# Optimization experiments

Measured on AMD Instinct MI355X. Metric: run time of the kernel, lower is better.

The kernel has to match this reference:

```python
import jax, jax.numpy as jnp
import numpy as np

N = 50000; E = 1600000; F_IN = 32; HEADS = 8; D = 16; HID = HEADS * D
ED = 16; G = 512; MH = 512; MO = 512; SLOPE = 0.2


def setup_inputs() -> dict:
    key = jax.random.key(0)
    ks = jax.random.split(key, 40)
    inp = {}
    inp["x"] = jax.random.normal(ks[0], (N, F_IN), jnp.float32)
    inp["edge_index"] = jax.random.randint(ks[1], (2, E), 0, N)
    inp["edge_attr"] = jax.random.normal(ks[2], (E, ED), jnp.float32)
    inp["batch"] = jnp.sort(jax.random.randint(ks[3], (N,), 0, G))

    def lin(k, fi, fo):
        return jax.random.normal(k, (fi, fo), jnp.float32) / np.sqrt(fi).astype(np.float32)

    i = 4
    dims = [(F_IN, HID), (HID, HID), (HID, HID)]  # GATv2 layers 0..2
    for l, (fi, fo) in enumerate(dims):
        inp[f"Wl{l}"] = lin(ks[i], fi, fo); i += 1
        inp[f"bl{l}"] = jnp.zeros((fo,), jnp.float32)
        inp[f"Wr{l}"] = lin(ks[i], fi, fo); i += 1
        inp[f"br{l}"] = jnp.zeros((fo,), jnp.float32)
        inp[f"We{l}"] = lin(ks[i], ED, fo); i += 1
        inp[f"att{l}"] = jax.random.normal(ks[i], (HEADS, D), jnp.float32) / np.sqrt(D).astype(np.float32); i += 1
        inp[f"b{l}"] = jnp.zeros((fo,), jnp.float32)
    inp["mW1"] = lin(ks[i], HID, MH); i += 1
    inp["mb1"] = jnp.zeros((MH,), jnp.float32)
    inp["ln_g"] = jnp.ones((MH,), jnp.float32)
    inp["ln_b"] = jnp.zeros((MH,), jnp.float32)
    inp["mW2"] = lin(ks[i], MH, MO); i += 1
    inp["mb2"] = jnp.zeros((MO,), jnp.float32)
    return inp


def _gatv2(h, src, dst, ea, Wl, bl, Wr, br, We, att, b):
    # One GATv2Conv layer (eval mode, add_self_loops already applied).
    n = h.shape[0]
    xl = (h @ Wl + bl).reshape(n, HEADS, D)   # source transform
    xr = (h @ Wr + br).reshape(n, HEADS, D)   # target transform
    ee = (ea @ We).reshape(-1, HEADS, D)      # edge transform (no bias in PyG)
    m = xl[src] + xr[dst] + ee                # [E', H, D]
    m = jnp.where(m > 0, m, SLOPE * m)        # LeakyReLU(0.2)
    s = jnp.einsum('ehd,hd->eh', m, att)      # attention logits
    mx = jax.ops.segment_max(s, dst, num_segments=n)
    ex = jnp.exp(s - mx[dst])
    den = jax.ops.segment_sum(ex, dst, num_segments=n)
    alpha = ex / den[dst]                     # softmax over incoming edges
    out = jax.ops.segment_sum(alpha[:, :, None] * xl[src], dst, num_segments=n)
    return out.reshape(n, HEADS * D) + b


def _forward(x, edge_index, edge_attr, batch,
             Wl0, bl0, Wr0, br0, We0, att0, b0,
             Wl1, bl1, Wr1, br1, We1, att1, b1,
             Wl2, bl2, Wr2, br2, We2, att2, b2,
             mW1, mb1, ln_g, ln_b, mW2, mb2):
    src, dst = edge_index[0], edge_index[1]
    # add_self_loops with fill_value='mean': self-loop edge_attr = mean of incoming edge_attr
    cnt = jax.ops.segment_sum(jnp.ones((E,), jnp.float32), dst, num_segments=N)
    loop_attr = jax.ops.segment_sum(edge_attr, dst, num_segments=N) / jnp.clip(cnt, 1.0)[:, None]
    nodes = jnp.arange(N)
    src_f = jnp.concatenate([src, nodes])
    dst_f = jnp.concatenate([dst, nodes])
    ea = jnp.concatenate([edge_attr, loop_attr], axis=0)

    h = jax.nn.relu(_gatv2(x, src_f, dst_f, ea, Wl0, bl0, Wr0, br0, We0, att0, b0))
    h = jax.nn.relu(_gatv2(h, src_f, dst_f, ea, Wl1, bl1, Wr1, br1, We1, att1, b1))
    h = _gatv2(h, src_f, dst_f, ea, Wl2, bl2, Wr2, br2, We2, att2, b2)

    g = jax.ops.segment_sum(h, batch, num_segments=G)  # sum pooling per graph
    z = jax.nn.relu(g @ mW1 + mb1)
    mu = jnp.mean(z, axis=-1, keepdims=True)
    var = jnp.var(z, axis=-1, keepdims=True)
    z = (z - mu) / jnp.sqrt(var + 1e-5) * ln_g + ln_b
    return z @ mW2 + mb2


def reference(x, edge_index, edge_attr, batch,
              Wl0, bl0, Wr0, br0, We0, att0, b0,
              Wl1, bl1, Wr1, br1, We1, att1, b1,
              Wl2, bl2, Wr2, br2, We2, att2, b2,
              mW1, mb1, ln_g, ln_b, mW2, mb2):
    return _forward(x, edge_index, edge_attr, batch,
                    Wl0, bl0, Wr0, br0, We0, att0, b0,
                    Wl1, bl1, Wr1, br1, We1, att1, b1,
                    Wl2, bl2, Wr2, br2, We2, att2, b2,
                    mW1, mb1, ln_g, ln_b, mW2, mb2)
```

## Files before the change

kernel.cpp:

```cpp
#include <hip/hip_runtime.h>
#include <math.h>

#define NN 50000
#define EE 1600000
#define FIN 32
#define HID_ 128
#define ED_ 16
#define GG 512
#define MH_ 512
#define MO_ 512

typedef float v2f __attribute__((ext_vector_type(2)));

#if __has_builtin(__builtin_amdgcn_exp2f)
#define EXP2(x) __builtin_amdgcn_exp2f(x)
#else
#define EXP2(x) exp2f(x)
#endif

template <int CTRL>
__device__ __forceinline__ float dpp_add(float x) {
  int m = __builtin_amdgcn_update_dpp(0, __float_as_int(x), CTRL, 0xF, 0xF, true);
  return x + __int_as_float(m);
}

__device__ __forceinline__ float bfly8(float p) {
  p = dpp_add<0xB1>(p);
  p = dpp_add<0x4E>(p);
  p = dpp_add<0x141>(p);
  return p;
}


__global__ void hist_kernel(const int4* __restrict__ dst4, int* __restrict__ cnt) {
  int e = blockIdx.x * 256 + threadIdx.x;
  if (e >= EE / 4) return;
  int4 d = dst4[e];
  atomicAdd(&cnt[d.x], 1);
  atomicAdd(&cnt[d.y], 1);
  atomicAdd(&cnt[d.z], 1);
  atomicAdd(&cnt[d.w], 1);
}

__global__ __launch_bounds__(256) void scan1_kernel(const int* __restrict__ in, int n,
                                                    int* __restrict__ out,
                                                    int* __restrict__ bsums) {
  int chunk = blockIdx.x;
  int base = chunk * 1024;
  int t = threadIdx.x;
  int idx = base + t * 4;
  int v0 = (idx + 0 < n) ? in[idx + 0] : 0;
  int v1 = (idx + 1 < n) ? in[idx + 1] : 0;
  int v2 = (idx + 2 < n) ? in[idx + 2] : 0;
  int v3 = (idx + 3 < n) ? in[idx + 3] : 0;
  int ts = v0 + v1 + v2 + v3;
  int lane = t & 63, w = t >> 6;
  int s = ts;
#pragma unroll
  for (int off = 1; off < 64; off <<= 1) {
    int o = __shfl_up(s, off);
    if (lane >= off) s += o;
  }
  __shared__ int wsum[4];
  if (lane == 63) wsum[w] = s;
  __syncthreads();
  int woff = 0;
  for (int i = 0; i < w; i++) woff += wsum[i];
  int excl = woff + s - ts;
  int run = excl;
  run += v0; if (idx + 0 < n) out[idx + 0] = run;
  run += v1; if (idx + 1 < n) out[idx + 1] = run;
  run += v2; if (idx + 2 < n) out[idx + 2] = run;
  run += v3; if (idx + 3 < n) out[idx + 3] = run;
  if (t == 255) bsums[chunk] = woff + s;
}

__global__ void scan_add_kernel(int* __restrict__ rowptr, const int* __restrict__ bscan, int n) {
  int i = blockIdx.x * 256 + threadIdx.x;
  if (i == 0) rowptr[0] = 0;
  if (i < n) {
    int chunk = i >> 10;
    if (chunk > 0) rowptr[1 + i] += bscan[chunk - 1];
  }
}

__global__ void scatter_kernel(const int4* __restrict__ src4, const int4* __restrict__ dst4,
                               const int* __restrict__ rowptr, int* __restrict__ fill,
                               int2* __restrict__ csr) {
  int e = blockIdx.x * 256 + threadIdx.x;
  if (e >= EE / 4) return;
  int4 s = src4[e];
  int4 d = dst4[e];
  int eb = e * 4;
  int p0 = rowptr[d.x] + atomicAdd(&fill[d.x], 1);
  csr[p0] = make_int2(s.x, eb + 0);
  int p1 = rowptr[d.y] + atomicAdd(&fill[d.y], 1);
  csr[p1] = make_int2(s.y, eb + 1);
  int p2 = rowptr[d.z] + atomicAdd(&fill[d.z], 1);
  csr[p2] = make_int2(s.z, eb + 2);
  int p3 = rowptr[d.w] + atomicAdd(&fill[d.w], 1);
  csr[p3] = make_int2(s.w, eb + 3);
}

__global__ __launch_bounds__(256) void loopattr_kernel(const int* __restrict__ rowptr,
                                                       const int2* __restrict__ csr,
                                                       const float* __restrict__ ea,
                                                       float* __restrict__ la) {
  int wid = threadIdx.x >> 6, lane = threadIdx.x & 63;
  int v = __builtin_amdgcn_readfirstlane(blockIdx.x * 4 + wid);
  if (v >= NN) return;
  int s = __builtin_amdgcn_readfirstlane(rowptr[v]);
  int e = __builtin_amdgcn_readfirstlane(rowptr[v + 1]);
  int k = lane >> 4;
  int d = lane & 15;
  float acc = 0.f;
  for (int j = s + k; j < e; j += 4) acc += ea[(size_t)csr[j].y * 16 + d];
  acc += __shfl_xor(acc, 16);
  acc += __shfl_xor(acc, 32);
  if (lane < 16) la[(size_t)v * 16 + d] = (e > s) ? acc / (float)(e - s) : 0.f;
}


template <int F>
__global__ __launch_bounds__(256) void node_transform(const float* __restrict__ h,
                                                      const float* __restrict__ Wlm,
                                                      const float* __restrict__ blm,
                                                      const float* __restrict__ Wrm,
                                                      const float* __restrict__ brm,
                                                      float* __restrict__ xl,
                                                      float* __restrict__ xr, int nnodes) {
  __shared__ float hs[F * 32];
  int v0 = blockIdx.x * 32;
  int t = threadIdx.x;
  for (int idx = t; idx < 32 * F; idx += 256) {
    int i = idx / F, k = idx - i * F;
    hs[k * 32 + i] = (v0 + i < nnodes) ? h[(size_t)(v0 + i) * F + k] : 0.f;
  }
  __syncthreads();
  bool isL = t < 128;
  int q = t & 63;
  int nh = (t >> 6) & 1;
  const float* Wm = isL ? Wlm : Wrm;
  v2f acc[16];
#pragma unroll
  for (int i = 0; i < 16; i++) acc[i] = (v2f){0.f, 0.f};
  for (int k = 0; k < F; k++) {
    v2f w = *(const v2f*)(Wm + k * 128 + 2 * q);
    const float4* hk4 = (const float4*)(hs + k * 32 + nh * 16);
#pragma unroll
    for (int r = 0; r < 4; r++) {
      float4 hv = hk4[r];
      acc[4 * r + 0] = __builtin_elementwise_fma((v2f){hv.x, hv.x}, w, acc[4 * r + 0]);
      acc[4 * r + 1] = __builtin_elementwise_fma((v2f){hv.y, hv.y}, w, acc[4 * r + 1]);
      acc[4 * r + 2] = __builtin_elementwise_fma((v2f){hv.z, hv.z}, w, acc[4 * r + 2]);
      acc[4 * r + 3] = __builtin_elementwise_fma((v2f){hv.w, hv.w}, w, acc[4 * r + 3]);
    }
  }
  const float* bm = isL ? blm : brm;
  v2f b = *(const v2f*)(bm + 2 * q);
  float* dstp = isL ? xl : xr;
  int base = v0 + nh * 16;
#pragma unroll
  for (int i = 0; i < 16; i++) {
    if (base + i < nnodes)
      *(v2f*)(dstp + (size_t)(base + i) * 128 + 2 * q) = acc[i] + b;
  }
}


__global__ __launch_bounds__(256) void gat_aggregate(
    const float* __restrict__ xl, const float* __restrict__ xr,
    const int* __restrict__ rowptr, const int2* __restrict__ csr,
    const float* __restrict__ ea, const float* __restrict__ la,
    const float* __restrict__ We, const float* __restrict__ att,
    const float* __restrict__ bias, float* __restrict__ hout, int relu) {
  int wid = threadIdx.x >> 6, lane = threadIdx.x & 63;
  int v = __builtin_amdgcn_readfirstlane(blockIdx.x * 4 + wid);
  if (v >= NN) return;
  int c = 2 * lane;
  v2f wec[16];
#pragma unroll
  for (int k = 0; k < 16; k++) wec[k] = *(const v2f*)(We + k * 128 + c);
  const float L2E = 1.44269504088896340736f;
  v2f av = *(const v2f*)(att + c) * L2E;
  v2f xrv = *(const v2f*)(xr + (size_t)v * 128 + c);

  auto score = [&](int u, const float* eaP, v2f& xu) -> float {
    xu = *(const v2f*)(xl + (size_t)u * 128 + c);
    v2f m = xrv + xu;
#pragma unroll
    for (int k = 0; k < 16; k++) {
      float e = eaP[k];
      m = __builtin_elementwise_fma((v2f){e, e}, wec[k], m);
    }
    m = __builtin_elementwise_max(m, 0.2f * m);
    v2f qq = av * m;
    return bfly8(qq.x + qq.y);
  };

  v2f acc;
  float den;
  {
    v2f xu;
    float p = score(v, la + (size_t)v * 16, xu);
    float w = EXP2(p);
    den = w;
    acc = (v2f){w, w} * xu;
  }
  int start = __builtin_amdgcn_readfirstlane(rowptr[v]);
  int end = __builtin_amdgcn_readfirstlane(rowptr[v + 1]);
  int j = start;
  for (; j + 4 <= end; j += 4) {
    int2 e0 = csr[j], e1 = csr[j + 1], e2 = csr[j + 2], e3 = csr[j + 3];
    int u0 = __builtin_amdgcn_readfirstlane(e0.x);
    int u1 = __builtin_amdgcn_readfirstlane(e1.x);
    int u2 = __builtin_amdgcn_readfirstlane(e2.x);
    int u3 = __builtin_amdgcn_readfirstlane(e3.x);
    const float* p0 = ea + (size_t)__builtin_amdgcn_readfirstlane(e0.y) * 16;
    const float* p1 = ea + (size_t)__builtin_amdgcn_readfirstlane(e1.y) * 16;
    const float* p2 = ea + (size_t)__builtin_amdgcn_readfirstlane(e2.y) * 16;
    const float* p3 = ea + (size_t)__builtin_amdgcn_readfirstlane(e3.y) * 16;
    v2f x0, x1, x2, x3;
    float s0 = score(u0, p0, x0);
    float s1 = score(u1, p1, x1);
    float s2 = score(u2, p2, x2);
    float s3 = score(u3, p3, x3);
    float w0 = EXP2(s0), w1 = EXP2(s1), w2 = EXP2(s2), w3 = EXP2(s3);
    den += (w0 + w1) + (w2 + w3);
    acc = __builtin_elementwise_fma((v2f){w0, w0}, x0,
          __builtin_elementwise_fma((v2f){w1, w1}, x1,
          __builtin_elementwise_fma((v2f){w2, w2}, x2,
          __builtin_elementwise_fma((v2f){w3, w3}, x3, acc))));
  }
  for (; j < end; ++j) {
    int2 e0 = csr[j];
    int u = __builtin_amdgcn_readfirstlane(e0.x);
    const float* p0 = ea + (size_t)__builtin_amdgcn_readfirstlane(e0.y) * 16;
    v2f xu;
    float p = score(u, p0, xu);
    float w = EXP2(p);
    den += w;
    acc = __builtin_elementwise_fma((v2f){w, w}, xu, acc);
  }
  float invd = 1.f / den;
  v2f bv = *(const v2f*)(bias + c);
  v2f o = __builtin_elementwise_fma(acc, (v2f){invd, invd}, bv);
  if (relu) o = __builtin_elementwise_max(o, (v2f){0.f, 0.f});
  *(v2f*)(hout + (size_t)v * 128 + c) = o;
}


__global__ void gptr_kernel(const int* __restrict__ batch, int* __restrict__ gptr) {
  int g = blockIdx.x * 256 + threadIdx.x;
  if (g > GG) return;
  int lo = 0, hi = NN;
  while (lo < hi) {
    int mid = (lo + hi) >> 1;
    if (batch[mid] < g) lo = mid + 1; else hi = mid;
  }
  gptr[g] = lo;
}

__global__ void pool_kernel(const float* __restrict__ h, const int* __restrict__ gptr,
                            float* __restrict__ gp) {
  int gi = blockIdx.x;
  int c = threadIdx.x;
  int s = gptr[gi], e = gptr[gi + 1];
  float acc = 0.f;
  for (int v = s; v < e; v++) acc += h[(size_t)v * 128 + c];
  gp[gi * 128 + c] = acc;
}

__global__ __launch_bounds__(256) void mlp1_kernel(const float* __restrict__ gp,
                                                   const float* __restrict__ mW1,
                                                   const float* __restrict__ mb1,
                                                   const float* __restrict__ lng,
                                                   const float* __restrict__ lnb,
                                                   float* __restrict__ z) {
  int row = blockIdx.x;
  int t = threadIdx.x;
  __shared__ float gs[128];
  if (t < 128) gs[t] = gp[row * 128 + t];
  __syncthreads();
  int c0 = t, c1 = t + 256;
  float z0 = 0.f, z1 = 0.f;
  for (int k = 0; k < 128; k++) {
    float gk = gs[k];
    z0 = fmaf(gk, mW1[k * 512 + c0], z0);
    z1 = fmaf(gk, mW1[k * 512 + c1], z1);
  }
  z0 += mb1[c0]; z1 += mb1[c1];
  z0 = fmaxf(z0, 0.f); z1 = fmaxf(z1, 0.f);
  float s = z0 + z1, q = z0 * z0 + z1 * z1;
#pragma unroll
  for (int off = 32; off > 0; off >>= 1) {
    s += __shfl_xor(s, off);
    q += __shfl_xor(q, off);
  }
  __shared__ float red[8];
  int lane = t & 63, w = t >> 6;
  if (lane == 0) { red[w] = s; red[4 + w] = q; }
  __syncthreads();
  float S = red[0] + red[1] + red[2] + red[3];
  float Q = red[4] + red[5] + red[6] + red[7];
  float mu = S / 512.f;
  float var = Q / 512.f - mu * mu;
  float inv = 1.f / sqrtf(var + 1e-5f);
  z[row * 512 + c0] = (z0 - mu) * inv * lng[c0] + lnb[c0];
  z[row * 512 + c1] = (z1 - mu) * inv * lng[c1] + lnb[c1];
}

__global__ __launch_bounds__(256) void mlp2_kernel(const float* __restrict__ z,
                                                   const float* __restrict__ mW2,
                                                   const float* __restrict__ mb2,
                                                   float* __restrict__ out) {
  int row = blockIdx.x;
  int t = threadIdx.x;
  __shared__ float zs[512];
  for (int i = t; i < 512; i += 256) zs[i] = z[row * 512 + i];
  __syncthreads();
  int c0 = t, c1 = t + 256;
  float o0 = 0.f, o1 = 0.f;
  for (int k = 0; k < 512; k++) {
    float zk = zs[k];
    o0 = fmaf(zk, mW2[k * 512 + c0], o0);
    o1 = fmaf(zk, mW2[k * 512 + c1], o1);
  }
  out[row * 512 + c0] = o0 + mb2[c0];
  out[row * 512 + c1] = o1 + mb2[c1];
}


extern "C" void kernel_launch(void* const* d_in, const int* in_sizes, int n_in,
                              void* d_out, int out_size, void* d_ws, size_t ws_size,
                              hipStream_t stream) {
  const float* x = (const float*)d_in[0];
  const int* ei = (const int*)d_in[1];
  const int* srcE = ei;
  const int* dstE = ei + EE;
  const float* ea = (const float*)d_in[2];
  const int* batch = (const int*)d_in[3];
  const float* Wl[3] = {(const float*)d_in[4], (const float*)d_in[11], (const float*)d_in[18]};
  const float* bl[3] = {(const float*)d_in[5], (const float*)d_in[12], (const float*)d_in[19]};
  const float* Wr[3] = {(const float*)d_in[6], (const float*)d_in[13], (const float*)d_in[20]};
  const float* br[3] = {(const float*)d_in[7], (const float*)d_in[14], (const float*)d_in[21]};
  const float* Wek[3] = {(const float*)d_in[8], (const float*)d_in[15], (const float*)d_in[22]};
  const float* attk[3] = {(const float*)d_in[9], (const float*)d_in[16], (const float*)d_in[23]};
  const float* bk[3] = {(const float*)d_in[10], (const float*)d_in[17], (const float*)d_in[24]};
  const float* mW1 = (const float*)d_in[25];
  const float* mb1 = (const float*)d_in[26];
  const float* lng = (const float*)d_in[27];
  const float* lnb = (const float*)d_in[28];
  const float* mW2 = (const float*)d_in[29];
  const float* mb2 = (const float*)d_in[30];
  float* outp = (float*)d_out;

  char* W = (char*)d_ws;
  size_t off = 0;
  auto take = [&](size_t b) -> void* {
    void* p = W + off;
    off += (b + 255) & ~(size_t)255;
    return p;
  };
  int* cnt = (int*)take(NN * 4);
  int* rowptr = (int*)take((NN + 1) * 4);
  int* bsums = (int*)take(64 * 4);
  int* bscan = (int*)take(64 * 4);
  int* dummy = (int*)take(64 * 4);
  int2* csr = (int2*)take((size_t)EE * 8);
  float* la = (float*)take((size_t)NN * 16 * 4);
  float* xl = (float*)take((size_t)NN * HID_ * 4);
  float* xr = (float*)take((size_t)NN * HID_ * 4);
  float* hbuf = (float*)take((size_t)NN * HID_ * 4);
  int* gptr = (int*)take((GG + 1) * 4);
  float* gpool = (float*)take((size_t)GG * HID_ * 4);
  float* z = (float*)take((size_t)GG * MH_ * 4);
  (void)ws_size; (void)n_in; (void)in_sizes; (void)out_size;

  hipMemsetAsync(cnt, 0, NN * 4, stream);
  hist_kernel<<<(EE / 4 + 255) / 256, 256, 0, stream>>>((const int4*)dstE, cnt);
  scan1_kernel<<<49, 256, 0, stream>>>(cnt, NN, rowptr + 1, bsums);
  scan1_kernel<<<1, 256, 0, stream>>>(bsums, 49, bscan, dummy);
  scan_add_kernel<<<(NN + 255) / 256, 256, 0, stream>>>(rowptr, bscan, NN);
  hipMemsetAsync(cnt, 0, NN * 4, stream);
  scatter_kernel<<<(EE / 4 + 255) / 256, 256, 0, stream>>>((const int4*)srcE, (const int4*)dstE,
                                                           rowptr, cnt, csr);
  loopattr_kernel<<<(NN + 3) / 4, 256, 0, stream>>>(rowptr, csr, ea, la);

  for (int l = 0; l < 3; l++) {
    if (l == 0)
      node_transform<FIN><<<(NN + 31) / 32, 256, 0, stream>>>(x, Wl[0], bl[0], Wr[0], br[0],
                                                              xl, xr, NN);
    else
      node_transform<HID_><<<(NN + 31) / 32, 256, 0, stream>>>(hbuf, Wl[l], bl[l], Wr[l], br[l],
                                                               xl, xr, NN);
    gat_aggregate<<<(NN + 3) / 4, 256, 0, stream>>>(xl, xr, rowptr, csr, ea, la,
                                                    Wek[l], attk[l], bk[l], hbuf,
                                                    (l < 2) ? 1 : 0);
  }

  gptr_kernel<<<3, 256, 0, stream>>>(batch, gptr);
  pool_kernel<<<GG, 128, 0, stream>>>(hbuf, gptr, gpool);
  mlp1_kernel<<<GG, 256, 0, stream>>>(gpool, mW1, mb1, lng, lnb, z);
  mlp2_kernel<<<GG, 256, 0, stream>>>(z, mW2, mb2, outp);
}
```

Baseline: 1.013 ms.

## Fuse self-loop edge-attribute mean into first GAT aggregation layer

Removes the separate loopattr kernel. The first-layer aggregation now accumulates the mean of incoming edge attributes while it walks each node's edges, then scores the self-loop last using that mean, which is broadcast via readlane. Later layers read the stored mean. The change also splits the packed v2f math into scalar float arrays and adds asm register pins. This saves one full pass over the CSR and edge attributes, at the cost of extra loads in layer 0 and a different register and instruction schedule.

```diff
diff --git a/kernel.cpp b/kernel.cpp
--- a/kernel.cpp
+++ b/kernel.cpp
@@ -102,24 +102,6 @@
   csr[p3] = make_int2(s.w, eb + 3);
 }
 
-__global__ __launch_bounds__(256) void loopattr_kernel(const int* __restrict__ rowptr,
-                                                       const int2* __restrict__ csr,
-                                                       const float* __restrict__ ea,
-                                                       float* __restrict__ la) {
-  int wid = threadIdx.x >> 6, lane = threadIdx.x & 63;
-  int v = __builtin_amdgcn_readfirstlane(blockIdx.x * 4 + wid);
-  if (v >= NN) return;
-  int s = __builtin_amdgcn_readfirstlane(rowptr[v]);
-  int e = __builtin_amdgcn_readfirstlane(rowptr[v + 1]);
-  int k = lane >> 4;
-  int d = lane & 15;
-  float acc = 0.f;
-  for (int j = s + k; j < e; j += 4) acc += ea[(size_t)csr[j].y * 16 + d];
-  acc += __shfl_xor(acc, 16);
-  acc += __shfl_xor(acc, 32);
-  if (lane < 16) la[(size_t)v * 16 + d] = (e > s) ? acc / (float)(e - s) : 0.f;
-}
-
 
 template <int F>
 __global__ __launch_bounds__(256) void node_transform(const float* __restrict__ h,
@@ -168,45 +150,55 @@
 }
 
 
+template <int LAYER0>
 __global__ __launch_bounds__(256) void gat_aggregate(
     const float* __restrict__ xl, const float* __restrict__ xr,
     const int* __restrict__ rowptr, const int2* __restrict__ csr,
-    const float* __restrict__ ea, const float* __restrict__ la,
+    const float* __restrict__ ea, float* __restrict__ la,
     const float* __restrict__ We, const float* __restrict__ att,
     const float* __restrict__ bias, float* __restrict__ hout, int relu) {
   int wid = threadIdx.x >> 6, lane = threadIdx.x & 63;
   int v = __builtin_amdgcn_readfirstlane(blockIdx.x * 4 + wid);
   if (v >= NN) return;
   int c = 2 * lane;
-  v2f wec[16];
-#pragma unroll
-  for (int k = 0; k < 16; k++) wec[k] = *(const v2f*)(We + k * 128 + c);
+  float wx[16], wy[16];
+#pragma unroll
+  for (int k = 0; k < 16; k++) {
+    wx[k] = We[k * 128 + c];
+    wy[k] = We[k * 128 + c + 1];
+  }
+#pragma unroll
+  for (int k = 0; k < 16; k++) {
+    asm volatile("" : "+v"(wx[k]));
+    asm volatile("" : "+v"(wy[k]));
+  }
   const float L2E = 1.44269504088896340736f;
-  v2f av = *(const v2f*)(att + c) * L2E;
+  float ax = att[c] * L2E, ay = att[c + 1] * L2E;
   v2f xrv = *(const v2f*)(xr + (size_t)v * 128 + c);
+  float xrx = xrv.x, xry = xrv.y;
+  asm volatile("" : "+v"(ax));
+  asm volatile("" : "+v"(ay));
+  asm volatile("" : "+v"(xrx));
+  asm volatile("" : "+v"(xry));
 
   auto score = [&](int u, const float* eaP, v2f& xu) -> float {
     xu = *(const v2f*)(xl + (size_t)u * 128 + c);
-    v2f m = xrv + xu;
+    float mx = xrx + xu.x, my = xry + xu.y;
 #pragma unroll
     for (int k = 0; k < 16; k++) {
       float e = eaP[k];
-      m = __builtin_elementwise_fma((v2f){e, e}, wec[k], m);
+      mx = fmaf(e, wx[k], mx);
+      my = fmaf(e, wy[k], my);
     }
-    m = __builtin_elementwise_max(m, 0.2f * m);
-    v2f qq = av * m;
-    return bfly8(qq.x + qq.y);
+    mx = fmaxf(mx, 0.2f * mx);
+    my = fmaxf(my, 0.2f * my);
+    return bfly8(fmaf(ax, mx, ay * my));
   };
 
-  v2f acc;
-  float den;
-  {
-    v2f xu;
-    float p = score(v, la + (size_t)v * 16, xu);
-    float w = EXP2(p);
-    den = w;
-    acc = (v2f){w, w} * xu;
-  }
+  int d16 = lane & 15;
+  v2f acc = (v2f){0.f, 0.f};
+  float den = 0.f;
+  float la_f = 0.f;
   int start = __builtin_amdgcn_readfirstlane(rowptr[v]);
   int end = __builtin_amdgcn_readfirstlane(rowptr[v + 1]);
   int j = start;
@@ -220,6 +212,7 @@
     const float* p1 = ea + (size_t)__builtin_amdgcn_readfirstlane(e1.y) * 16;
     const float* p2 = ea + (size_t)__builtin_amdgcn_readfirstlane(e2.y) * 16;
     const float* p3 = ea + (size_t)__builtin_amdgcn_readfirstlane(e3.y) * 16;
+    if (LAYER0) la_f += (p0[d16] + p1[d16]) + (p2[d16] + p3[d16]);
     v2f x0, x1, x2, x3;
     float s0 = score(u0, p0, x0);
     float s1 = score(u1, p1, x1);
@@ -236,12 +229,39 @@
     int2 e0 = csr[j];
     int u = __builtin_amdgcn_readfirstlane(e0.x);
     const float* p0 = ea + (size_t)__builtin_amdgcn_readfirstlane(e0.y) * 16;
+    if (LAYER0) la_f += p0[d16];
     v2f xu;
     float p = score(u, p0, xu);
     float w = EXP2(p);
     den += w;
     acc = __builtin_elementwise_fma((v2f){w, w}, xu, acc);
   }
+
+  int deg = end - start;
+  if (LAYER0) {
+    float invdeg = (deg > 0) ? 1.f / (float)deg : 0.f;
+    la_f *= invdeg;
+    if (lane < 16) la[(size_t)v * 16 + d16] = la_f;
+  } else {
+    la_f = la[(size_t)v * 16 + d16];
+  }
+  {
+    v2f xu = *(const v2f*)(xl + (size_t)v * 128 + c);
+    float mx = xrx + xu.x, my = xry + xu.y;
+#pragma unroll
+    for (int k = 0; k < 16; k++) {
+      float e = __int_as_float(__builtin_amdgcn_readlane(__float_as_int(la_f), k));
+      mx = fmaf(e, wx[k], mx);
+      my = fmaf(e, wy[k], my);
+    }
+    mx = fmaxf(mx, 0.2f * mx);
+    my = fmaxf(my, 0.2f * my);
+    float p = bfly8(fmaf(ax, mx, ay * my));
+    float w = EXP2(p);
+    den += w;
+    acc = __builtin_elementwise_fma((v2f){w, w}, xu, acc);
+  }
+
   float invd = 1.f / den;
   v2f bv = *(const v2f*)(bias + c);
   v2f o = __builtin_elementwise_fma(acc, (v2f){invd, invd}, bv);
@@ -385,7 +405,6 @@
   hipMemsetAsync(cnt, 0, NN * 4, stream);
   scatter_kernel<<<(EE / 4 + 255) / 256, 256, 0, stream>>>((const int4*)srcE, (const int4*)dstE,
                                                            rowptr, cnt, csr);
-  loopattr_kernel<<<(NN + 3) / 4, 256, 0, stream>>>(rowptr, csr, ea, la);
 
   for (int l = 0; l < 3; l++) {
     if (l == 0)
@@ -394,9 +413,13 @@
     else
       node_transform<HID_><<<(NN + 31) / 32, 256, 0, stream>>>(hbuf, Wl[l], bl[l], Wr[l], br[l],
                                                                xl, xr, NN);
-    gat_aggregate<<<(NN + 3) / 4, 256, 0, stream>>>(xl, xr, rowptr, csr, ea, la,
-                                                    Wek[l], attk[l], bk[l], hbuf,
-                                                    (l < 2) ? 1 : 0);
+    if (l == 0)
+      gat_aggregate<1><<<(NN + 3) / 4, 256, 0, stream>>>(xl, xr, rowptr, csr, ea, la,
+                                                         Wek[0], attk[0], bk[0], hbuf, 1);
+    else
+      gat_aggregate<0><<<(NN + 3) / 4, 256, 0, stream>>>(xl, xr, rowptr, csr, ea, la,
+                                                         Wek[l], attk[l], bk[l], hbuf,
+                                                         (l < 2) ? 1 : 0);
   }
 
   gptr_kernel<<<3, 256, 0, stream>>>(batch, gptr);
```

New measurement: 961.2 us. -5.1%, faster.

## Fuse loop-attr mean into histogram via float atomics; pad node_transform LDS

Applied to the files above, without the earlier changes.

Self-loop edge attributes are now computed as a per-node mean by float atomics inside the histogram pass, followed by a small normalize kernel. This replaces the separate CSR-gather kernel that read edge_attr through the edge permutation. Separately, node_transform pads its shared-memory tile stride from 32 to 34 and reads it with 8-byte loads to cut bank conflicts. The trade is about 25.6M float atomics spread over 800K addresses, and atomic ordering makes the summation order nondeterministic.

```diff
diff --git a/kernel.cpp b/kernel.cpp
--- a/kernel.cpp
+++ b/kernel.cpp
@@ -32,14 +32,32 @@
 }
 
 
-__global__ void hist_kernel(const int4* __restrict__ dst4, int* __restrict__ cnt) {
+__global__ void hist_la_kernel(const int* __restrict__ dst, const float4* __restrict__ ea4,
+                               int* __restrict__ cnt, float* __restrict__ laS) {
   int e = blockIdx.x * 256 + threadIdx.x;
-  if (e >= EE / 4) return;
-  int4 d = dst4[e];
-  atomicAdd(&cnt[d.x], 1);
-  atomicAdd(&cnt[d.y], 1);
-  atomicAdd(&cnt[d.z], 1);
-  atomicAdd(&cnt[d.w], 1);
+  if (e >= EE) return;
+  int v = dst[e];
+  atomicAdd(&cnt[v], 1);
+  float* lp = laS + (size_t)v * 16;
+  float4 q0 = ea4[e * 4 + 0], q1 = ea4[e * 4 + 1];
+  float4 q2 = ea4[e * 4 + 2], q3 = ea4[e * 4 + 3];
+  atomicAdd(lp + 0, q0.x);  atomicAdd(lp + 1, q0.y);
+  atomicAdd(lp + 2, q0.z);  atomicAdd(lp + 3, q0.w);
+  atomicAdd(lp + 4, q1.x);  atomicAdd(lp + 5, q1.y);
+  atomicAdd(lp + 6, q1.z);  atomicAdd(lp + 7, q1.w);
+  atomicAdd(lp + 8, q2.x);  atomicAdd(lp + 9, q2.y);
+  atomicAdd(lp + 10, q2.z); atomicAdd(lp + 11, q2.w);
+  atomicAdd(lp + 12, q3.x); atomicAdd(lp + 13, q3.y);
+  atomicAdd(lp + 14, q3.z); atomicAdd(lp + 15, q3.w);
+}
+
+__global__ void norm_la_kernel(const float* __restrict__ laS, const int* __restrict__ cnt,
+                               float* __restrict__ la) {
+  int t = blockIdx.x * 256 + threadIdx.x;
+  if (t >= NN * 16) return;
+  int v = t >> 4;
+  int d = cnt[v];
+  la[t] = (d > 0) ? laS[t] / (float)d : 0.f;
 }
 
 __global__ __launch_bounds__(256) void scan1_kernel(const int* __restrict__ in, int n,
@@ -102,24 +120,6 @@
   csr[p3] = make_int2(s.w, eb + 3);
 }
 
-__global__ __launch_bounds__(256) void loopattr_kernel(const int* __restrict__ rowptr,
-                                                       const int2* __restrict__ csr,
-                                                       const float* __restrict__ ea,
-                                                       float* __restrict__ la) {
-  int wid = threadIdx.x >> 6, lane = threadIdx.x & 63;
-  int v = __builtin_amdgcn_readfirstlane(blockIdx.x * 4 + wid);
-  if (v >= NN) return;
-  int s = __builtin_amdgcn_readfirstlane(rowptr[v]);
-  int e = __builtin_amdgcn_readfirstlane(rowptr[v + 1]);
-  int k = lane >> 4;
-  int d = lane & 15;
-  float acc = 0.f;
-  for (int j = s + k; j < e; j += 4) acc += ea[(size_t)csr[j].y * 16 + d];
-  acc += __shfl_xor(acc, 16);
-  acc += __shfl_xor(acc, 32);
-  if (lane < 16) la[(size_t)v * 16 + d] = (e > s) ? acc / (float)(e - s) : 0.f;
-}
-
 
 template <int F>
 __global__ __launch_bounds__(256) void node_transform(const float* __restrict__ h,
@@ -129,12 +129,12 @@
                                                       const float* __restrict__ brm,
                                                       float* __restrict__ xl,
                                                       float* __restrict__ xr, int nnodes) {
-  __shared__ float hs[F * 32];
+  __shared__ float hs[F * 34];
   int v0 = blockIdx.x * 32;
   int t = threadIdx.x;
   for (int idx = t; idx < 32 * F; idx += 256) {
     int i = idx / F, k = idx - i * F;
-    hs[k * 32 + i] = (v0 + i < nnodes) ? h[(size_t)(v0 + i) * F + k] : 0.f;
+    hs[k * 34 + i] = (v0 + i < nnodes) ? h[(size_t)(v0 + i) * F + k] : 0.f;
   }
   __syncthreads();
   bool isL = t < 128;
@@ -146,14 +146,12 @@
   for (int i = 0; i < 16; i++) acc[i] = (v2f){0.f, 0.f};
   for (int k = 0; k < F; k++) {
     v2f w = *(const v2f*)(Wm + k * 128 + 2 * q);
-    const float4* hk4 = (const float4*)(hs + k * 32 + nh * 16);
-#pragma unroll
-    for (int r = 0; r < 4; r++) {
-      float4 hv = hk4[r];
-      acc[4 * r + 0] = __builtin_elementwise_fma((v2f){hv.x, hv.x}, w, acc[4 * r + 0]);
-      acc[4 * r + 1] = __builtin_elementwise_fma((v2f){hv.y, hv.y}, w, acc[4 * r + 1]);
-      acc[4 * r + 2] = __builtin_elementwise_fma((v2f){hv.z, hv.z}, w, acc[4 * r + 2]);
-      acc[4 * r + 3] = __builtin_elementwise_fma((v2f){hv.w, hv.w}, w, acc[4 * r + 3]);
+    const v2f* hk2 = (const v2f*)(hs + k * 34 + nh * 16);
+#pragma unroll
+    for (int r = 0; r < 8; r++) {
+      v2f hv = hk2[r];
+      acc[2 * r + 0] = __builtin_elementwise_fma((v2f){hv.x, hv.x}, w, acc[2 * r + 0]);
+      acc[2 * r + 1] = __builtin_elementwise_fma((v2f){hv.y, hv.y}, w, acc[2 * r + 1]);
     }
   }
   const float* bm = isL ? blm : brm;
@@ -368,6 +366,7 @@
   int* bscan = (int*)take(64 * 4);
   int* dummy = (int*)take(64 * 4);
   int2* csr = (int2*)take((size_t)EE * 8);
+  float* laS = (float*)take((size_t)NN * 16 * 4);
   float* la = (float*)take((size_t)NN * 16 * 4);
   float* xl = (float*)take((size_t)NN * HID_ * 4);
   float* xr = (float*)take((size_t)NN * HID_ * 4);
@@ -378,14 +377,15 @@
   (void)ws_size; (void)n_in; (void)in_sizes; (void)out_size;
 
   hipMemsetAsync(cnt, 0, NN * 4, stream);
-  hist_kernel<<<(EE / 4 + 255) / 256, 256, 0, stream>>>((const int4*)dstE, cnt);
+  hipMemsetAsync(laS, 0, (size_t)NN * 16 * 4, stream);
+  hist_la_kernel<<<(EE + 255) / 256, 256, 0, stream>>>(dstE, (const float4*)ea, cnt, laS);
   scan1_kernel<<<49, 256, 0, stream>>>(cnt, NN, rowptr + 1, bsums);
   scan1_kernel<<<1, 256, 0, stream>>>(bsums, 49, bscan, dummy);
   scan_add_kernel<<<(NN + 255) / 256, 256, 0, stream>>>(rowptr, bscan, NN);
+  norm_la_kernel<<<(NN * 16 + 255) / 256, 256, 0, stream>>>(laS, cnt, la);
   hipMemsetAsync(cnt, 0, NN * 4, stream);
   scatter_kernel<<<(EE / 4 + 255) / 256, 256, 0, stream>>>((const int4*)srcE, (const int4*)dstE,
                                                            rowptr, cnt, csr);
-  loopattr_kernel<<<(NN + 3) / 4, 256, 0, stream>>>(rowptr, csr, ea, la);
 
   for (int l = 0; l < 3; l++) {
     if (l == 0)
```

Measured after the change: 2.259 ms. 123% more time.
